# Performance work log

Measured on AMD Instinct MI355X. Metric: run time of the kernel, lower is better.

## Reference

```python
import jax, jax.numpy as jnp
import numpy as np

GROUPS = 32
EPS = 1e-5


def setup_inputs() -> dict:
    key = jax.random.key(0)
    ks = jax.random.split(key, 6)
    B, H, W, C = 2, 64, 64, 512
    wscale = 0.02  # keep logits in a sane range for softmax
    return {
        "x": jax.random.normal(ks[0], (B, H, W, C), dtype=jnp.float32),
        "gamma": jnp.ones((C,), jnp.float32),
        "beta": jnp.zeros((C,), jnp.float32),
        "wq": jax.random.normal(ks[1], (C, C), dtype=jnp.float32) * wscale,
        "bq": jnp.zeros((C,), jnp.float32),
        "wk": jax.random.normal(ks[2], (C, C), dtype=jnp.float32) * wscale,
        "bk": jnp.zeros((C,), jnp.float32),
        "wv": jax.random.normal(ks[3], (C, C), dtype=jnp.float32) * wscale,
        "bv": jnp.zeros((C,), jnp.float32),
        "wp": jax.random.normal(ks[4], (C, C), dtype=jnp.float32) * wscale,
        "bp": jnp.zeros((C,), jnp.float32),
    }


def _group_norm(x, gamma, beta):
    B, H, W, C = x.shape
    xg = x.reshape(B, H, W, GROUPS, C // GROUPS)
    mean = xg.mean(axis=(1, 2, 4), keepdims=True)
    var = xg.var(axis=(1, 2, 4), keepdims=True)
    xn = ((xg - mean) * jax.lax.rsqrt(var + EPS)).reshape(B, H, W, C)
    return xn * gamma + beta


def reference(x, gamma, beta, wq, bq, wk, bk, wv, bv, wp, bp):
    B, H, W, C = x.shape
    xn = _group_norm(x, gamma, beta)
    # 1x1 convs == per-pixel linear layers
    q = (xn @ wq + bq).reshape(B, H * W, C)
    k = (xn @ wk + bk).reshape(B, H * W, C)
    v = (xn @ wv + bv).reshape(B, H * W, C)
    scale = C ** (-0.5)
    attn = jax.nn.softmax(jnp.einsum("bqc,bkc->bqk", q, k) * scale, axis=-1)
    out = jnp.einsum("bqk,bkc->bqc", attn, v).reshape(B, H, W, C)
    return (out @ wp + bp) + x
```

## Files before the change

kernel.cpp:

```cpp
#include <hip/hip_runtime.h>


typedef __bf16 bf16_t;
typedef __bf16 bf16x8 __attribute__((ext_vector_type(8)));
typedef __bf16 bf16x4 __attribute__((ext_vector_type(4)));
typedef float  f32x4  __attribute__((ext_vector_type(4)));

__device__ __forceinline__ bf16x8 ld8(const bf16_t* p) {
    return *reinterpret_cast<const bf16x8*>(p);
}
__device__ __forceinline__ f32x4 mfma16(bf16x8 a, bf16x8 b, f32x4 c) {
    return __builtin_amdgcn_mfma_f32_16x16x32_bf16(a, b, c, 0, 0, 0);
}
__device__ __forceinline__ void gload16(const bf16_t* gp, bf16_t* lp) {
    __builtin_amdgcn_global_load_lds(
        (const __attribute__((address_space(1))) void*)gp,
        (__attribute__((address_space(3))) void*)lp, 16, 0, 0);
}

#define NPIX 8192
#define C512 512
#define SEQ  4096
#define QSCALE 0.044194173824159216f

__global__ __launch_bounds__(256) void gn_stats_k(const float* __restrict__ x,
                                                  float* __restrict__ stats) {
    int bg = blockIdx.x;
    int b  = bg >> 5, g = bg & 31;
    const float* xp = x + (size_t)b * SEQ * C512 + g * 16;
    float s = 0.f, s2 = 0.f;
    for (int p = threadIdx.x; p < SEQ; p += 256) {
        const float4* q = reinterpret_cast<const float4*>(xp + (size_t)p * C512);
        #pragma unroll
        for (int i = 0; i < 4; i++) {
            float4 v = q[i];
            s  += v.x + v.y + v.z + v.w;
            s2 += v.x*v.x + v.y*v.y + v.z*v.z + v.w*v.w;
        }
    }
    #pragma unroll
    for (int off = 32; off >= 1; off >>= 1) {
        s  += __shfl_down(s, off);
        s2 += __shfl_down(s2, off);
    }
    __shared__ float rs[4], rs2[4];
    int wave = threadIdx.x >> 6;
    if ((threadIdx.x & 63) == 0) { rs[wave] = s; rs2[wave] = s2; }
    __syncthreads();
    if (threadIdx.x == 0) {
        float S = 0.f, S2 = 0.f;
        for (int i = 0; i < 4; i++) { S += rs[i]; S2 += rs2[i]; }
        float mean = S * (1.f / 65536.f);
        float var  = S2 * (1.f / 65536.f) - mean * mean;
        stats[bg * 2]     = mean;
        stats[bg * 2 + 1] = rsqrtf(var + 1e-5f);
    }
}

__global__ __launch_bounds__(256) void wt_conv_k(const float* wq, const float* wk,
                                                 const float* wv, const float* wp,
                                                 bf16_t* wqkvT, bf16_t* wpT) {
    int y = blockIdx.y;
    const float* w = (y == 0) ? wq : (y == 1) ? wk : (y == 2) ? wv : wp;
    float scale = (y == 0) ? QSCALE : 1.0f;
    int tid = blockIdx.x * 256 + threadIdx.x;
    int n = tid >> 9, k = tid & 511;
    bf16_t val = (bf16_t)(w[(size_t)k * C512 + n] * scale);
    if (y < 3) wqkvT[((size_t)y * C512 + n) * C512 + k] = val;
    else       wpT[(size_t)n * C512 + k] = val;
}

__global__ __launch_bounds__(256) void bias_merge_k(const float* bq, const float* bk,
                                                    const float* bv, float* bqkv) {
    int i = blockIdx.x * 256 + threadIdx.x;
    float v = (i < 512) ? bq[i] * QSCALE : (i < 1024) ? bk[i - 512] : bv[i - 1024];
    bqkv[i] = v;
}

__global__ __launch_bounds__(256) void xn_k(const float* __restrict__ x,
                                            const float* __restrict__ stats,
                                            const float* __restrict__ gamma,
                                            const float* __restrict__ beta,
                                            bf16_t* __restrict__ xn) {
    size_t idx = ((size_t)blockIdx.x * 256 + threadIdx.x) * 4;
    int c = (int)(idx & 511);
    size_t pix = idx >> 9;
    int b = (int)(pix >> 12);
    int g = c >> 4;
    float mean = stats[(b * 32 + g) * 2];
    float rstd = stats[(b * 32 + g) * 2 + 1];
    float4 v  = *reinterpret_cast<const float4*>(x + idx);
    float4 gm = *reinterpret_cast<const float4*>(gamma + c);
    float4 bt = *reinterpret_cast<const float4*>(beta + c);
    bf16x4 o;
    o[0] = (bf16_t)((v.x - mean) * rstd * gm.x + bt.x);
    o[1] = (bf16_t)((v.y - mean) * rstd * gm.y + bt.y);
    o[2] = (bf16_t)((v.z - mean) * rstd * gm.z + bt.z);
    o[3] = (bf16_t)((v.w - mean) * rstd * gm.w + bt.w);
    *reinterpret_cast<bf16x4*>(xn + idx) = o;
}

template <int MODE>
__global__ __launch_bounds__(256, 2) void gemm128_k(
        const bf16_t* __restrict__ Aall, const bf16_t* __restrict__ Ball,
        const float* __restrict__ bias, const float* __restrict__ resid,
        void* __restrict__ out0, void* __restrict__ out1,
        void* __restrict__ out2, void* __restrict__ out3,
        float* __restrict__ lsum) {
    __shared__ bf16_t as_[2][4096];
    __shared__ bf16_t bs_[2][4096];

    int lane = threadIdx.x & 63;
    int w    = threadIdx.x >> 6;
    int wr   = w >> 1, wc = w & 1;
    int lrow = lane & 15, quad = lane >> 4;
    int bz   = blockIdx.z;

    const bf16_t* A;
    const bf16_t* B;
    size_t lda, ldb;
    int ksteps, kofs = 0, zb = bz, sp = 0;
    if (MODE == 0)      { A = Aall;                         B = Ball;                        lda = 512;  ldb = 512;  ksteps = 16; }
    else if (MODE == 1) { A = Aall + (size_t)bz*SEQ*C512;   B = Ball + (size_t)bz*SEQ*C512;  lda = 512;  ldb = 512;  ksteps = 16; }
    else if (MODE == 2) { zb = bz >> 2; sp = bz & 3;
                          A = Aall + (size_t)zb*SEQ*SEQ;    B = Ball + (size_t)zb*C512*SEQ;  lda = SEQ;  ldb = SEQ;  ksteps = 32; kofs = sp * 1024; }
    else                { A = Aall;                         B = Ball;                        lda = 512;  ldb = 512;  ksteps = 16; }

    int bm = blockIdx.x * 128, bn = blockIdx.y * 128;

    auto stage = [&](int buf, int ks) {
        size_t k0 = (size_t)kofs + (size_t)ks * 32;
        #pragma unroll
        for (int ii = 0; ii < 2; ii++) {
            int c = w * 2 + ii;
            const bf16_t* gpA = A + (size_t)(bm + c * 16 + lrow) * lda + k0 + quad * 8;
            gload16(gpA, &as_[buf][c * 512]);
            const bf16_t* gpB = B + (size_t)(bn + c * 16 + lrow) * ldb + k0 + quad * 8;
            gload16(gpB, &bs_[buf][c * 512]);
        }
    };

    f32x4 acc[4][4] = {};

    stage(0, 0);

    for (int ks = 0; ks < ksteps; ks++) {
        int cur = ks & 1;
        __syncthreads();
        if (ks + 1 < ksteps) stage(1 - cur, ks + 1);

        const bf16_t* al = &as_[cur][(wr * 4) * 512];
        const bf16_t* bl = &bs_[cur][(wc * 4) * 512];
        bf16x8 af[4], bf[4];
        #pragma unroll
        for (int m = 0; m < 4; m++) af[m] = ld8(al + m * 512 + lane * 8);
        #pragma unroll
        for (int n = 0; n < 4; n++) bf[n] = ld8(bl + n * 512 + lane * 8);
        #pragma unroll
        for (int m = 0; m < 4; m++)
            #pragma unroll
            for (int n = 0; n < 4; n++)
                acc[m][n] = mfma16(af[m], bf[n], acc[m][n]);
    }

    float rs[4][4];
    if (MODE == 1) {
        #pragma unroll
        for (int m = 0; m < 4; m++)
            #pragma unroll
            for (int i = 0; i < 4; i++) rs[m][i] = 0.f;
    }

    #pragma unroll
    for (int m = 0; m < 4; m++) {
        int rowb = bm + wr * 64 + m * 16 + quad * 4;
        #pragma unroll
        for (int n = 0; n < 4; n++) {
            int col = bn + wc * 64 + n * 16 + lrow;
            #pragma unroll
            for (int i = 0; i < 4; i++) {
                int row = rowb + i;
                float v = acc[m][n][i];
                if (MODE == 0) {
                    int seg = col >> 9, c = col & 511;
                    bf16_t val = (bf16_t)(v + bias[col]);
                    if (seg == 0) {
                        ((bf16_t*)out0)[(size_t)row * C512 + c] = val;
                    } else if (seg == 1) {
                        ((bf16_t*)out1)[(size_t)row * C512 + c] = val;
                    } else {
                        int b = row >> 12, s = row & 4095;
                        ((bf16_t*)out2)[((size_t)(b * C512 + c)) * SEQ + s] = val;
                    }
                } else if (MODE == 1) {
                    float p = __expf(fminf(v, 20.0f));
                    bf16_t* P = (bf16_t*)out0 + (size_t)bz * SEQ * SEQ;
                    P[(size_t)row * SEQ + col] = (bf16_t)p;
                    rs[m][i] += p;
                } else if (MODE == 2) {
                    bf16_t* Ops = (bf16_t*)((sp == 0) ? out0 : (sp == 1) ? out1
                                          : (sp == 2) ? out2 : out3);
                    Ops[((size_t)zb * SEQ + row) * C512 + col] = (bf16_t)v;
                } else {
                    size_t idx = (size_t)row * C512 + col;
                    ((float*)out0)[idx] = v + bias[col] + resid[idx];
                }
            }
        }
    }

    if (MODE == 1) {
        #pragma unroll
        for (int m = 0; m < 4; m++) {
            #pragma unroll
            for (int i = 0; i < 4; i++) {
                float r = rs[m][i];
                r += __shfl_xor(r, 1);
                r += __shfl_xor(r, 2);
                r += __shfl_xor(r, 4);
                r += __shfl_xor(r, 8);
                if (lrow == 0) {
                    int row = bm + wr * 64 + m * 16 + quad * 4 + i;
                    atomicAdd(&lsum[(size_t)bz * SEQ + row], r);
                }
            }
        }
    }
}

__global__ __launch_bounds__(256) void attn_combine_k(const bf16_t* __restrict__ Op0,
                                                      const bf16_t* __restrict__ Op1,
                                                      const bf16_t* __restrict__ Op2,
                                                      const bf16_t* __restrict__ Op3,
                                                      const float* __restrict__ lsum,
                                                      bf16_t* __restrict__ O) {
    int idx = blockIdx.x * 256 + threadIdx.x;
    int row = idx >> 6;
    int c8  = (idx & 63) << 3;
    float inv = 1.0f / lsum[row];
    size_t base = (size_t)row * C512 + c8;
    bf16x8 o0 = ld8(Op0 + base), o1 = ld8(Op1 + base);
    bf16x8 o2 = ld8(Op2 + base), o3 = ld8(Op3 + base);
    bf16x8 o;
    #pragma unroll
    for (int j = 0; j < 8; j++)
        o[j] = (bf16_t)(((float)o0[j] + (float)o1[j] +
                         (float)o2[j] + (float)o3[j]) * inv);
    *reinterpret_cast<bf16x8*>(O + base) = o;
}

extern "C" void kernel_launch(void* const* d_in, const int* in_sizes, int n_in,
                              void* d_out, int out_size, void* d_ws, size_t ws_size,
                              hipStream_t stream) {
    const float* x     = (const float*)d_in[0];
    const float* gamma = (const float*)d_in[1];
    const float* beta  = (const float*)d_in[2];
    const float* wq = (const float*)d_in[3];  const float* bq = (const float*)d_in[4];
    const float* wk = (const float*)d_in[5];  const float* bk = (const float*)d_in[6];
    const float* wv = (const float*)d_in[7];  const float* bv = (const float*)d_in[8];
    const float* wp = (const float*)d_in[9];  const float* bp = (const float*)d_in[10];
    float* out = (float*)d_out;

    char* ws = (char*)d_ws;
    size_t off = 0;
    float*  stats  = (float*)(ws + off);   off += 1024;
    float*  bqkv   = (float*)(ws + off);   off += 1536 * sizeof(float);
    float*  lsum   = (float*)(ws + off);   off += (size_t)NPIX * sizeof(float);
    bf16_t* xn     = (bf16_t*)(ws + off);  off += (size_t)NPIX * C512 * 2;
    bf16_t* wqkvT  = (bf16_t*)(ws + off);  off += (size_t)3 * C512 * C512 * 2;
    bf16_t* wpT    = (bf16_t*)(ws + off);  off += (size_t)C512 * C512 * 2;
    bf16_t* Qb     = (bf16_t*)(ws + off);  off += (size_t)NPIX * C512 * 2;
    bf16_t* Kb     = (bf16_t*)(ws + off);  off += (size_t)NPIX * C512 * 2;
    bf16_t* VTb    = (bf16_t*)(ws + off);  off += (size_t)NPIX * C512 * 2;
    bf16_t* Op2    = (bf16_t*)(ws + off);  off += (size_t)NPIX * C512 * 2;
    bf16_t* Op3    = (bf16_t*)(ws + off);  off += (size_t)NPIX * C512 * 2;
    bf16_t* P      = (bf16_t*)(ws + off);  off += (size_t)2 * SEQ * SEQ * 2;
    bf16_t* Ob  = xn;
    bf16_t* Op0 = Qb;
    bf16_t* Op1 = Kb;

    hipMemsetAsync(lsum, 0, (size_t)NPIX * sizeof(float), stream);

    gn_stats_k<<<64, 256, 0, stream>>>(x, stats);
    wt_conv_k<<<dim3(1024, 4), 256, 0, stream>>>(wq, wk, wv, wp, wqkvT, wpT);
    bias_merge_k<<<6, 256, 0, stream>>>(bq, bk, bv, bqkv);
    xn_k<<<4096, 256, 0, stream>>>(x, stats, gamma, beta, xn);

    gemm128_k<0><<<dim3(64, 12, 1), 256, 0, stream>>>(
        xn, wqkvT, bqkv, nullptr, Qb, Kb, VTb, nullptr, nullptr);

    gemm128_k<1><<<dim3(32, 32, 2), 256, 0, stream>>>(
        Qb, Kb, nullptr, nullptr, P, nullptr, nullptr, nullptr, lsum);

    gemm128_k<2><<<dim3(32, 4, 8), 256, 0, stream>>>(
        P, VTb, nullptr, nullptr, Op0, Op1, Op2, Op3, nullptr);

    attn_combine_k<<<2048, 256, 0, stream>>>(Op0, Op1, Op2, Op3, lsum, Ob);

    gemm128_k<3><<<dim3(64, 4, 1), 256, 0, stream>>>(
        Ob, wpT, bp, x, out, nullptr, nullptr, nullptr, nullptr);
}
```

Baseline: 320.5 us.

## Split GN stats across blocks, stage P tile via LDS, shrink proj GEMM tile

Group-norm statistics are now computed by 512 blocks that atomically accumulate sums, with mean and rstd finished inside xn_k, so the single 64-block reduction no longer serialises. In the QK^T GEMM, the exponentiated scores are staged through shared memory and written to P as coalesced 16-byte rows instead of scattered 2-byte stores. The output projection uses 64-row tiles to double its grid from 256 to 512 blocks. The costs are extra atomics, redundant rstd math per thread, and one extra shared-memory round trip with a barrier in the score epilogue.

```diff
diff --git a/kernel.cpp b/kernel.cpp
--- a/kernel.cpp
+++ b/kernel.cpp
@@ -23,13 +23,16 @@
 #define SEQ  4096
 #define QSCALE 0.044194173824159216f
 
-__global__ __launch_bounds__(256) void gn_stats_k(const float* __restrict__ x,
-                                                  float* __restrict__ stats) {
-    int bg = blockIdx.x;
-    int b  = bg >> 5, g = bg & 31;
+__global__ __launch_bounds__(256) void gn_sum_k(const float* __restrict__ x,
+                                                float* __restrict__ accum) {
+    int bg    = blockIdx.x >> 3;
+    int slice = blockIdx.x & 7;
+    int b = bg >> 5, g = bg & 31;
     const float* xp = x + (size_t)b * SEQ * C512 + g * 16;
     float s = 0.f, s2 = 0.f;
-    for (int p = threadIdx.x; p < SEQ; p += 256) {
+    #pragma unroll
+    for (int pp = 0; pp < 2; pp++) {
+        int p = slice * 512 + pp * 256 + threadIdx.x;
         const float4* q = reinterpret_cast<const float4*>(xp + (size_t)p * C512);
         #pragma unroll
         for (int i = 0; i < 4; i++) {
@@ -48,12 +51,10 @@
     if ((threadIdx.x & 63) == 0) { rs[wave] = s; rs2[wave] = s2; }
     __syncthreads();
     if (threadIdx.x == 0) {
-        float S = 0.f, S2 = 0.f;
-        for (int i = 0; i < 4; i++) { S += rs[i]; S2 += rs2[i]; }
-        float mean = S * (1.f / 65536.f);
-        float var  = S2 * (1.f / 65536.f) - mean * mean;
-        stats[bg * 2]     = mean;
-        stats[bg * 2 + 1] = rsqrtf(var + 1e-5f);
+        float S = rs[0] + rs[1] + rs[2] + rs[3];
+        float S2 = rs2[0] + rs2[1] + rs2[2] + rs2[3];
+        atomicAdd(&accum[bg * 2],     S);
+        atomicAdd(&accum[bg * 2 + 1], S2);
     }
 }
 
@@ -78,7 +79,7 @@
 }
 
 __global__ __launch_bounds__(256) void xn_k(const float* __restrict__ x,
-                                            const float* __restrict__ stats,
+                                            const float* __restrict__ accum,
                                             const float* __restrict__ gamma,
                                             const float* __restrict__ beta,
                                             bf16_t* __restrict__ xn) {
@@ -87,8 +88,11 @@
     size_t pix = idx >> 9;
     int b = (int)(pix >> 12);
     int g = c >> 4;
-    float mean = stats[(b * 32 + g) * 2];
-    float rstd = stats[(b * 32 + g) * 2 + 1];
+    float sum = accum[(b * 32 + g) * 2];
+    float ssq = accum[(b * 32 + g) * 2 + 1];
+    float mean = sum * (1.f / 65536.f);
+    float var  = ssq * (1.f / 65536.f) - mean * mean;
+    float rstd = rsqrtf(var + 1e-5f);
     float4 v  = *reinterpret_cast<const float4*>(x + idx);
     float4 gm = *reinterpret_cast<const float4*>(gamma + c);
     float4 bt = *reinterpret_cast<const float4*>(beta + c);
@@ -107,8 +111,12 @@
         void* __restrict__ out0, void* __restrict__ out1,
         void* __restrict__ out2, void* __restrict__ out3,
         float* __restrict__ lsum) {
-    __shared__ bf16_t as_[2][4096];
-    __shared__ bf16_t bs_[2][4096];
+    constexpr int TM  = (MODE == 3) ? 64 : 128;
+    constexpr int ASZ = TM * 32;
+    constexpr int ACH = TM / 16;
+    constexpr int CPW = (ACH + 8) / 4;
+    constexpr int MI  = TM / 32;
+    __shared__ bf16_t smem[2 * ASZ + 8192];
 
     int lane = threadIdx.x & 63;
     int w    = threadIdx.x >> 6;
@@ -126,21 +134,25 @@
                           A = Aall + (size_t)zb*SEQ*SEQ;    B = Ball + (size_t)zb*C512*SEQ;  lda = SEQ;  ldb = SEQ;  ksteps = 32; kofs = sp * 1024; }
     else                { A = Aall;                         B = Ball;                        lda = 512;  ldb = 512;  ksteps = 16; }
 
-    int bm = blockIdx.x * 128, bn = blockIdx.y * 128;
+    int bm = blockIdx.x * TM, bn = blockIdx.y * 128;
 
     auto stage = [&](int buf, int ks) {
         size_t k0 = (size_t)kofs + (size_t)ks * 32;
         #pragma unroll
-        for (int ii = 0; ii < 2; ii++) {
-            int c = w * 2 + ii;
-            const bf16_t* gpA = A + (size_t)(bm + c * 16 + lrow) * lda + k0 + quad * 8;
-            gload16(gpA, &as_[buf][c * 512]);
-            const bf16_t* gpB = B + (size_t)(bn + c * 16 + lrow) * ldb + k0 + quad * 8;
-            gload16(gpB, &bs_[buf][c * 512]);
+        for (int ii = 0; ii < CPW; ii++) {
+            int c = w * CPW + ii;
+            if (c < ACH) {
+                const bf16_t* gpA = A + (size_t)(bm + c * 16 + lrow) * lda + k0 + quad * 8;
+                gload16(gpA, &smem[buf * ASZ + c * 512]);
+            } else {
+                int cb = c - ACH;
+                const bf16_t* gpB = B + (size_t)(bn + cb * 16 + lrow) * ldb + k0 + quad * 8;
+                gload16(gpB, &smem[2 * ASZ + buf * 4096 + cb * 512]);
+            }
         }
     };
 
-    f32x4 acc[4][4] = {};
+    f32x4 acc[MI][4] = {};
 
     stage(0, 0);
 
@@ -149,31 +161,71 @@
         __syncthreads();
         if (ks + 1 < ksteps) stage(1 - cur, ks + 1);
 
-        const bf16_t* al = &as_[cur][(wr * 4) * 512];
-        const bf16_t* bl = &bs_[cur][(wc * 4) * 512];
-        bf16x8 af[4], bf[4];
-        #pragma unroll
-        for (int m = 0; m < 4; m++) af[m] = ld8(al + m * 512 + lane * 8);
+        const bf16_t* al = &smem[cur * ASZ + (wr * MI) * 512];
+        const bf16_t* bl = &smem[2 * ASZ + cur * 4096 + (wc * 4) * 512];
+        bf16x8 af[MI], bf[4];
+        #pragma unroll
+        for (int m = 0; m < MI; m++) af[m] = ld8(al + m * 512 + lane * 8);
         #pragma unroll
         for (int n = 0; n < 4; n++) bf[n] = ld8(bl + n * 512 + lane * 8);
         #pragma unroll
-        for (int m = 0; m < 4; m++)
+        for (int m = 0; m < MI; m++)
             #pragma unroll
             for (int n = 0; n < 4; n++)
                 acc[m][n] = mfma16(af[m], bf[n], acc[m][n]);
     }
 
-    float rs[4][4];
     if (MODE == 1) {
+        __syncthreads();
+        float rs[4][4];
         #pragma unroll
         for (int m = 0; m < 4; m++)
             #pragma unroll
             for (int i = 0; i < 4; i++) rs[m][i] = 0.f;
+        #pragma unroll
+        for (int m = 0; m < MI; m++) {
+            #pragma unroll
+            for (int n = 0; n < 4; n++) {
+                #pragma unroll
+                for (int i = 0; i < 4; i++) {
+                    float p = __expf(fminf(acc[m][n][i], 20.0f));
+                    rs[m][i] += p;
+                    int row_l = wr * 64 + m * 16 + quad * 4 + i;
+                    int col_l = wc * 64 + n * 16 + lrow;
+                    smem[row_l * 128 + col_l] = (bf16_t)p;
+                }
+            }
+        }
+        __syncthreads();
+        bf16_t* Pg = (bf16_t*)out0 + (size_t)bz * SEQ * SEQ;
+        #pragma unroll
+        for (int k = 0; k < 8; k++) {
+            int chunk = k * 256 + threadIdx.x;
+            int row = chunk >> 4, c8 = (chunk & 15) * 8;
+            bf16x8 v = *reinterpret_cast<const bf16x8*>(&smem[row * 128 + c8]);
+            *reinterpret_cast<bf16x8*>(&Pg[(size_t)(bm + row) * SEQ + bn + c8]) = v;
+        }
+        #pragma unroll
+        for (int m = 0; m < MI; m++) {
+            #pragma unroll
+            for (int i = 0; i < 4; i++) {
+                float r = rs[m][i];
+                r += __shfl_xor(r, 1);
+                r += __shfl_xor(r, 2);
+                r += __shfl_xor(r, 4);
+                r += __shfl_xor(r, 8);
+                if (lrow == 0) {
+                    int row = bm + wr * 64 + m * 16 + quad * 4 + i;
+                    atomicAdd(&lsum[(size_t)bz * SEQ + row], r);
+                }
+            }
+        }
+        return;
     }
 
     #pragma unroll
-    for (int m = 0; m < 4; m++) {
-        int rowb = bm + wr * 64 + m * 16 + quad * 4;
+    for (int m = 0; m < MI; m++) {
+        int rowb = bm + wr * (TM / 2) + m * 16 + quad * 4;
         #pragma unroll
         for (int n = 0; n < 4; n++) {
             int col = bn + wc * 64 + n * 16 + lrow;
@@ -192,11 +244,6 @@
                         int b = row >> 12, s = row & 4095;
                         ((bf16_t*)out2)[((size_t)(b * C512 + c)) * SEQ + s] = val;
                     }
-                } else if (MODE == 1) {
-                    float p = __expf(fminf(v, 20.0f));
-                    bf16_t* P = (bf16_t*)out0 + (size_t)bz * SEQ * SEQ;
-                    P[(size_t)row * SEQ + col] = (bf16_t)p;
-                    rs[m][i] += p;
                 } else if (MODE == 2) {
                     bf16_t* Ops = (bf16_t*)((sp == 0) ? out0 : (sp == 1) ? out1
                                           : (sp == 2) ? out2 : out3);
@@ -204,24 +251,6 @@
                 } else {
                     size_t idx = (size_t)row * C512 + col;
                     ((float*)out0)[idx] = v + bias[col] + resid[idx];
-                }
-            }
-        }
-    }
-
-    if (MODE == 1) {
-        #pragma unroll
-        for (int m = 0; m < 4; m++) {
-            #pragma unroll
-            for (int i = 0; i < 4; i++) {
-                float r = rs[m][i];
-                r += __shfl_xor(r, 1);
-                r += __shfl_xor(r, 2);
-                r += __shfl_xor(r, 4);
-                r += __shfl_xor(r, 8);
-                if (lrow == 0) {
-                    int row = bm + wr * 64 + m * 16 + quad * 4 + i;
-                    atomicAdd(&lsum[(size_t)bz * SEQ + row], r);
                 }
             }
         }
@@ -263,9 +292,9 @@
 
     char* ws = (char*)d_ws;
     size_t off = 0;
-    float*  stats  = (float*)(ws + off);   off += 1024;
     float*  bqkv   = (float*)(ws + off);   off += 1536 * sizeof(float);
     float*  lsum   = (float*)(ws + off);   off += (size_t)NPIX * sizeof(float);
+    float*  accum  = (float*)(ws + off);   off += 128 * sizeof(float);
     bf16_t* xn     = (bf16_t*)(ws + off);  off += (size_t)NPIX * C512 * 2;
     bf16_t* wqkvT  = (bf16_t*)(ws + off);  off += (size_t)3 * C512 * C512 * 2;
     bf16_t* wpT    = (bf16_t*)(ws + off);  off += (size_t)C512 * C512 * 2;
@@ -279,12 +308,12 @@
     bf16_t* Op0 = Qb;
     bf16_t* Op1 = Kb;
 
-    hipMemsetAsync(lsum, 0, (size_t)NPIX * sizeof(float), stream);
-
-    gn_stats_k<<<64, 256, 0, stream>>>(x, stats);
+    hipMemsetAsync(lsum, 0, (size_t)(NPIX + 128) * sizeof(float), stream);
+
+    gn_sum_k<<<512, 256, 0, stream>>>(x, accum);
     wt_conv_k<<<dim3(1024, 4), 256, 0, stream>>>(wq, wk, wv, wp, wqkvT, wpT);
     bias_merge_k<<<6, 256, 0, stream>>>(bq, bk, bv, bqkv);
-    xn_k<<<4096, 256, 0, stream>>>(x, stats, gamma, beta, xn);
+    xn_k<<<4096, 256, 0, stream>>>(x, accum, gamma, beta, xn);
 
     gemm128_k<0><<<dim3(64, 12, 1), 256, 0, stream>>>(
         xn, wqkvT, bqkv, nullptr, Qb, Kb, VTb, nullptr, nullptr);
@@ -297,6 +326,6 @@
 
     attn_combine_k<<<2048, 256, 0, stream>>>(Op0, Op1, Op2, Op3, lsum, Ob);
 
-    gemm128_k<3><<<dim3(64, 4, 1), 256, 0, stream>>>(
+    gemm128_k<3><<<dim3(128, 4, 1), 256, 0, stream>>>(
         Ob, wpT, bp, x, out, nullptr, nullptr, nullptr, nullptr);
 }
```

After: 310.1 us. 3.2% less time.
